# Performance work log

Measured on AMD Instinct MI355X. Metric: run time of the kernel, lower is better.

Reference implementation:

```python
import jax, jax.numpy as jnp
import numpy as np

N = 50000   # nnodes
E = 1600000 # edges (avg degree 32)
F = 128     # nfeatures
D = 64      # output_dim
T = 10      # s2v iterations (default in n2v)


def setup_inputs() -> dict:
    key = jax.random.key(0)
    k_x, k_s, k_d, k_w1, k_w2 = jax.random.split(key, 5)
    x = jax.random.normal(k_x, (N, F), dtype=jnp.float32)
    edge_src = jax.random.randint(k_s, (E,), 0, N, dtype=jnp.int32)
    edge_dst = jax.random.randint(k_d, (E,), 0, N, dtype=jnp.int32)
    # xavier_uniform init as in reset_parameters
    s1 = float(np.sqrt(6.0 / (F + D)))
    s2 = float(np.sqrt(6.0 / (D + D)))
    W1 = jax.random.uniform(k_w1, (D, F), jnp.float32, -s1, s1)
    W2 = jax.random.uniform(k_w2, (D, D), jnp.float32, -s2, s2)
    b1 = jnp.zeros((D,), jnp.float32)
    b2 = jnp.zeros((D,), jnp.float32)
    return {"x": x, "W1": W1, "b1": b1, "W2": W2, "b2": b2,
            "edge_src": edge_src, "edge_dst": edge_dst}


def reference(x, W1, b1, W2, b2, edge_src, edge_dst):
    Wx = x @ W1.T + b1                      # [N, D]

    def step(emb, _):
        # sum of neighbor embeddings: gather sources, segment-sum into dests
        agg = jax.ops.segment_sum(emb[edge_src], edge_dst, num_segments=N)  # [N, D]
        emb_new = jax.nn.relu(Wx + agg @ W2.T + b2)
        return emb_new, None

    emb0 = jnp.zeros((N, D), dtype=x.dtype)
    emb, _ = jax.lax.scan(step, emb0, None, length=T)  # n2v
    # g2v: sum node embeddings into graph embedding
    return emb.sum(axis=0)                  # [D]
```

## Files before the change

### kernel.cpp

```cpp
#include <hip/hip_runtime.h>

#define D 64
#define F 128
#define NBMAX 256
#define DB 128

typedef unsigned int uint;
typedef unsigned short ushort;
typedef short s16x8 __attribute__((ext_vector_type(8)));
typedef float f32x4 __attribute__((ext_vector_type(4)));

__device__ __forceinline__ float bf16lo(uint u) { return __uint_as_float(u << 16); }
__device__ __forceinline__ float bf16hi(uint u) { return __uint_as_float(u & 0xFFFF0000u); }
__device__ __forceinline__ ushort f2bf16(float f) {
    uint u = __float_as_uint(f);
    u += 0x7FFFu + ((u >> 16) & 1u);
    return (ushort)(u >> 16);
}
__device__ __forceinline__ uint pk2bf(float lo, float hi) {
    return (uint)f2bf16(lo) | ((uint)f2bf16(hi) << 16);
}


__global__ __launch_bounds__(256) void bucket_hist(const int* __restrict__ dst,
                                                   int* __restrict__ gb, int E, int nb) {
    __shared__ int h[NBMAX];
    for (int t = threadIdx.x; t < nb; t += 256) h[t] = 0;
    __syncthreads();
    int start = blockIdx.x * 4096;
    int end   = start + 4096 < E ? start + 4096 : E;
    for (int i = start + threadIdx.x; i < end; i += 256)
        atomicAdd(&h[dst[i] >> 8], 1);
    __syncthreads();
    for (int t = threadIdx.x; t < nb; t += 256)
        if (h[t]) atomicAdd(&gb[t], h[t]);
}

__global__ void bucket_scan(const int* __restrict__ gb, int* __restrict__ gboff,
                            int* __restrict__ gcur, int nb) {
    if (threadIdx.x == 0) {
        int s = 0;
        for (int b = 0; b < nb; ++b) { gboff[b] = s; gcur[b] = s; s += gb[b]; }
        gboff[nb] = s;
    }
}

__global__ __launch_bounds__(256) void bucket_scatter(const int* __restrict__ src,
                                                      const int* __restrict__ dst,
                                                      int* __restrict__ gcur,
                                                      int* __restrict__ packed, int E, int nb) {
    __shared__ int h[NBMAX], base[NBMAX], lcur[NBMAX];
    for (int t = threadIdx.x; t < nb; t += 256) h[t] = 0;
    __syncthreads();
    int start = blockIdx.x * 4096;
    int end   = start + 4096 < E ? start + 4096 : E;
    for (int i = start + threadIdx.x; i < end; i += 256)
        atomicAdd(&h[dst[i] >> 8], 1);
    __syncthreads();
    for (int t = threadIdx.x; t < nb; t += 256) {
        base[t] = h[t] ? atomicAdd(&gcur[t], h[t]) : 0;
        lcur[t] = 0;
    }
    __syncthreads();
    for (int i = start + threadIdx.x; i < end; i += 256) {
        int d = dst[i];
        int b = d >> 8;
        int pos = base[b] + atomicAdd(&lcur[b], 1);
        packed[pos] = (src[i] << 8) | (d & 255);
    }
}

__global__ __launch_bounds__(256) void bucket_deg(const int* __restrict__ gboff,
                                                  const int* __restrict__ packed,
                                                  int* __restrict__ deg, int N) {
    __shared__ int h[NBMAX];
    int b = blockIdx.x;
    h[threadIdx.x] = 0;
    __syncthreads();
    int st = gboff[b], en = gboff[b + 1];
    for (int i = st + threadIdx.x; i < en; i += 256)
        atomicAdd(&h[packed[i] & 255], 1);
    __syncthreads();
    int node = (b << 8) + threadIdx.x;
    if (node < N) deg[node] = h[threadIdx.x];
}

__global__ __launch_bounds__(256) void bucket_fill(const int* __restrict__ gboff,
                                                   const int* __restrict__ packed,
                                                   const int* __restrict__ row_ptr,
                                                   const int* __restrict__ rank,
                                                   int* __restrict__ col, int N) {
    __shared__ int lcur[NBMAX];
    int b = blockIdx.x;
    int node = (b << 8) + threadIdx.x;
    lcur[threadIdx.x] = (node < N) ? row_ptr[node] : 0;
    __syncthreads();
    int st = gboff[b], en = gboff[b + 1];
    for (int i = st + threadIdx.x; i < en; i += 256) {
        int p = packed[i];
        int pos = atomicAdd(&lcur[p & 255], 1);
        col[pos] = rank[p >> 8];
    }
}


__global__ void count_deg_kernel(const int* __restrict__ dst, int* __restrict__ deg, int E) {
    int i = blockIdx.x * blockDim.x + threadIdx.x;
    if (i < E) atomicAdd(&deg[dst[i]], 1);
}

__global__ void fill_kernel(const int* __restrict__ src, const int* __restrict__ dst,
                            int* __restrict__ cursor, const int* __restrict__ rank,
                            int* __restrict__ col, int E) {
    int i = blockIdx.x * blockDim.x + threadIdx.x;
    if (i < E) {
        int d_ = dst[i];
        int pos = atomicAdd(&cursor[d_], 1);
        col[pos] = rank[src[i]];
    }
}


__global__ __launch_bounds__(256) void dsort_hist(const int* __restrict__ deg,
                                                  int* __restrict__ dh, int N) {
    __shared__ int h[DB];
    if (threadIdx.x < DB) h[threadIdx.x] = 0;
    __syncthreads();
    int start = blockIdx.x * 4096;
    int end   = start + 4096 < N ? start + 4096 : N;
    for (int i = start + threadIdx.x; i < end; i += 256) {
        int d = deg[i];
        atomicAdd(&h[d < DB - 1 ? d : DB - 1], 1);
    }
    __syncthreads();
    if (threadIdx.x < DB && h[threadIdx.x]) atomicAdd(&dh[threadIdx.x], h[threadIdx.x]);
}

__global__ void dsort_scan(const int* __restrict__ dh, int* __restrict__ dcur) {
    if (threadIdx.x == 0) {
        int s = 0;
        for (int b = 0; b < DB; ++b) { dcur[b] = s; s += dh[b]; }
    }
}

__global__ __launch_bounds__(256) void dsort_scatter(const int* __restrict__ deg,
                                                     int* __restrict__ dcur,
                                                     int* __restrict__ perm,
                                                     int* __restrict__ rank, int N) {
    __shared__ int h[DB], base[DB], lc[DB];
    if (threadIdx.x < DB) h[threadIdx.x] = 0;
    __syncthreads();
    int start = blockIdx.x * 4096;
    int end   = start + 4096 < N ? start + 4096 : N;
    for (int i = start + threadIdx.x; i < end; i += 256) {
        int d = deg[i];
        atomicAdd(&h[d < DB - 1 ? d : DB - 1], 1);
    }
    __syncthreads();
    if (threadIdx.x < DB) {
        base[threadIdx.x] = h[threadIdx.x] ? atomicAdd(&dcur[threadIdx.x], h[threadIdx.x]) : 0;
        lc[threadIdx.x] = 0;
    }
    __syncthreads();
    for (int i = start + threadIdx.x; i < end; i += 256) {
        int d = deg[i];
        int b = d < DB - 1 ? d : DB - 1;
        int pos = base[b] + atomicAdd(&lc[b], 1);
        perm[pos] = i;
        rank[i] = pos;
    }
}


__global__ __launch_bounds__(1024) void scan_kernel(const int* __restrict__ deg,
                                                    int* __restrict__ row_ptr, int n) {
    __shared__ int wsum[16];
    int lane = threadIdx.x & 63;
    int wid  = threadIdx.x >> 6;
    int carry = 0;
    const int CH = 4096;
    for (int base = 0; base < n; base += CH) {
        int i0 = base + (int)threadIdx.x * 4;
        int v0 = (i0     < n) ? deg[i0]     : 0;
        int v1 = (i0 + 1 < n) ? deg[i0 + 1] : 0;
        int v2 = (i0 + 2 < n) ? deg[i0 + 2] : 0;
        int v3 = (i0 + 3 < n) ? deg[i0 + 3] : 0;
        int p0 = v0, p1 = p0 + v1, p2 = p1 + v2, p3 = p2 + v3;
        int tsum = p3;
        int s = tsum;
        #pragma unroll
        for (int off = 1; off < 64; off <<= 1) {
            int t = __shfl_up(s, off);
            if (lane >= off) s += t;
        }
        if (lane == 63) wsum[wid] = s;
        __syncthreads();
        int wbase = 0, chunk_total = 0;
        #pragma unroll
        for (int w = 0; w < 16; ++w) {
            int t = wsum[w];
            chunk_total += t;
            if (w < wid) wbase += t;
        }
        __syncthreads();
        int ex = carry + wbase + (s - tsum);
        if (i0     < n) row_ptr[i0 + 1] = ex + p0;
        if (i0 + 1 < n) row_ptr[i0 + 2] = ex + p1;
        if (i0 + 2 < n) row_ptr[i0 + 3] = ex + p2;
        if (i0 + 3 < n) row_ptr[i0 + 4] = ex + p3;
        carry += chunk_total;
    }
    if (threadIdx.x == 0) row_ptr[0] = 0;
}


__global__ __launch_bounds__(256) void wx_mfma_kernel(const float* __restrict__ x,
                                                      const float* __restrict__ W1,
                                                      const float* __restrict__ b1,
                                                      const float* __restrict__ b2,
                                                      const int* __restrict__ perm,
                                                      float* __restrict__ Wx,
                                                      ushort* __restrict__ emb, int N) {
    int lane = threadIdx.x & 63;
    int wv = blockIdx.x * 4 + (threadIdx.x >> 6);
    int nwaves = gridDim.x * 4;
    int r16 = lane & 15;
    int kg  = lane >> 4;

    s16x8 bf[4][4];
    #pragma unroll
    for (int nt = 0; nt < 4; ++nt) {
        const float* wrow = W1 + (size_t)(nt * 16 + r16) * F;
        #pragma unroll
        for (int ks = 0; ks < 4; ++ks) {
            const float4* p = reinterpret_cast<const float4*>(wrow + ks * 32 + kg * 8);
            float4 f0 = p[0], f1 = p[1];
            union { s16x8 v; uint u[4]; } t;
            t.u[0] = pk2bf(f0.x, f0.y); t.u[1] = pk2bf(f0.z, f0.w);
            t.u[2] = pk2bf(f1.x, f1.y); t.u[3] = pk2bf(f1.z, f1.w);
            bf[nt][ks] = t.v;
        }
    }
    float b1v[4], b2v[4];
    #pragma unroll
    for (int nt = 0; nt < 4; ++nt) {
        b1v[nt] = b1[nt * 16 + r16];
        b2v[nt] = b2[nt * 16 + r16];
    }

    int ntiles = (N + 15) >> 4;
    for (int tile = wv; tile < ntiles; tile += nwaves) {
        int row0 = tile << 4;
        int arow = row0 + r16;
        if (arow >= N) arow = N - 1;
        int orig = perm[arow];
        s16x8 af[4];
        #pragma unroll
        for (int ks = 0; ks < 4; ++ks) {
            const float4* p = reinterpret_cast<const float4*>(x + (size_t)orig * F + ks * 32 + kg * 8);
            float4 f0 = p[0], f1 = p[1];
            union { s16x8 v; uint u[4]; } t;
            t.u[0] = pk2bf(f0.x, f0.y); t.u[1] = pk2bf(f0.z, f0.w);
            t.u[2] = pk2bf(f1.x, f1.y); t.u[3] = pk2bf(f1.z, f1.w);
            af[ks] = t.v;
        }
        #pragma unroll
        for (int nt = 0; nt < 4; ++nt) {
            f32x4 acc = {0.f, 0.f, 0.f, 0.f};
            #pragma unroll
            for (int ks = 0; ks < 4; ++ks)
                acc = __builtin_amdgcn_mfma_f32_16x16x32_bf16(af[ks], bf[nt][ks], acc, 0, 0, 0);
            int outd = nt * 16 + r16;
            #pragma unroll
            for (int r = 0; r < 4; ++r) {
                int node = row0 + kg * 4 + r;
                if (node < N) {
                    float wxv = acc[r] + b1v[nt];
                    Wx[(size_t)node * D + outd] = wxv;
                    float e = wxv + b2v[nt];
                    emb[(size_t)node * D + outd] = f2bf16(e > 0.f ? e : 0.f);
                }
            }
        }
    }
}


__global__ __launch_bounds__(256) void step_kernel(const ushort* __restrict__ emb_in,
                                                   ushort* __restrict__ emb_out,
                                                   const float* __restrict__ Wx,
                                                   const float* __restrict__ W2,
                                                   const float* __restrict__ b2,
                                                   const int* __restrict__ row_ptr,
                                                   const int* __restrict__ col,
                                                   const int* __restrict__ perm, int N) {
    int lane = threadIdx.x & 63;
    int w = threadIdx.x >> 6;
    int r = lane & 15;
    int a = lane >> 4;

    s16x8 af[4][2];
    #pragma unroll
    for (int t = 0; t < 4; ++t)
        #pragma unroll
        for (int f = 0; f < 2; ++f) {
            const float4* p = reinterpret_cast<const float4*>(W2 + (size_t)(t * 16 + r) * D + f * 32 + a * 8);
            float4 f0 = p[0], f1 = p[1];
            union { s16x8 v; uint u[4]; } tt;
            tt.u[0] = pk2bf(f0.x, f0.y); tt.u[1] = pk2bf(f0.z, f0.w);
            tt.u[2] = pk2bf(f1.x, f1.y); tt.u[3] = pk2bf(f1.z, f1.w);
            af[t][f] = tt.v;
        }
    float4 b2v[4];
    #pragma unroll
    for (int t = 0; t < 4; ++t)
        b2v[t] = *reinterpret_cast<const float4*>(b2 + t * 16 + a * 4);

    int ntiles = (N + 15) >> 4;
    int tile = blockIdx.x * 4 + w;
    if (tile >= ntiles) return;

    int rg = tile * 16 + r;
    int rgc = rg < N ? rg : N - 1;
    int node = perm[rgc];
    int rp = row_ptr[node];
    int degr = row_ptr[node + 1] - rp;
    if (rg >= N) degr = 0;
    int maxd = degr;
    #pragma unroll
    for (int off = 1; off < 16; off <<= 1) {
        int o = __shfl_xor(maxd, off);
        maxd = o > maxd ? o : maxd;
    }

    float acc0[8] = {0.f, 0.f, 0.f, 0.f, 0.f, 0.f, 0.f, 0.f};
    float acc1[8] = {0.f, 0.f, 0.f, 0.f, 0.f, 0.f, 0.f, 0.f};

    if (maxd > 0) {
        int u0 = (0 < degr) ? col[rp] : N;
        int u1 = (1 < degr) ? col[rp + 1] : N;
        uint4 q00 = *reinterpret_cast<const uint4*>(emb_in + ((size_t)u0 << 6) + (a << 3));
        uint4 q01 = *reinterpret_cast<const uint4*>(emb_in + ((size_t)u0 << 6) + 32 + (a << 3));
        uint4 q10 = *reinterpret_cast<const uint4*>(emb_in + ((size_t)u1 << 6) + (a << 3));
        uint4 q11 = *reinterpret_cast<const uint4*>(emb_in + ((size_t)u1 << 6) + 32 + (a << 3));
        for (int k = 0; k < maxd; ++k) {
            int un = (k + 2 < degr) ? col[rp + k + 2] : N;
            uint4 p0 = *reinterpret_cast<const uint4*>(emb_in + ((size_t)un << 6) + (a << 3));
            uint4 p1 = *reinterpret_cast<const uint4*>(emb_in + ((size_t)un << 6) + 32 + (a << 3));
            acc0[0] += bf16lo(q00.x); acc0[1] += bf16hi(q00.x);
            acc0[2] += bf16lo(q00.y); acc0[3] += bf16hi(q00.y);
            acc0[4] += bf16lo(q00.z); acc0[5] += bf16hi(q00.z);
            acc0[6] += bf16lo(q00.w); acc0[7] += bf16hi(q00.w);
            acc1[0] += bf16lo(q01.x); acc1[1] += bf16hi(q01.x);
            acc1[2] += bf16lo(q01.y); acc1[3] += bf16hi(q01.y);
            acc1[4] += bf16lo(q01.z); acc1[5] += bf16hi(q01.z);
            acc1[6] += bf16lo(q01.w); acc1[7] += bf16hi(q01.w);
            q00 = q10; q01 = q11; q10 = p0; q11 = p1;
        }
    }

    union { s16x8 v; uint u[4]; } B0, B1;
    B0.u[0] = pk2bf(acc0[0], acc0[1]); B0.u[1] = pk2bf(acc0[2], acc0[3]);
    B0.u[2] = pk2bf(acc0[4], acc0[5]); B0.u[3] = pk2bf(acc0[6], acc0[7]);
    B1.u[0] = pk2bf(acc1[0], acc1[1]); B1.u[1] = pk2bf(acc1[2], acc1[3]);
    B1.u[2] = pk2bf(acc1[4], acc1[5]); B1.u[3] = pk2bf(acc1[6], acc1[7]);

    f32x4 d0 = {0.f, 0.f, 0.f, 0.f}, d1 = {0.f, 0.f, 0.f, 0.f};
    f32x4 d2 = {0.f, 0.f, 0.f, 0.f}, d3 = {0.f, 0.f, 0.f, 0.f};
    d0 = __builtin_amdgcn_mfma_f32_16x16x32_bf16(af[0][0], B0.v, d0, 0, 0, 0);
    d1 = __builtin_amdgcn_mfma_f32_16x16x32_bf16(af[1][0], B0.v, d1, 0, 0, 0);
    d2 = __builtin_amdgcn_mfma_f32_16x16x32_bf16(af[2][0], B0.v, d2, 0, 0, 0);
    d3 = __builtin_amdgcn_mfma_f32_16x16x32_bf16(af[3][0], B0.v, d3, 0, 0, 0);
    d0 = __builtin_amdgcn_mfma_f32_16x16x32_bf16(af[0][1], B1.v, d0, 0, 0, 0);
    d1 = __builtin_amdgcn_mfma_f32_16x16x32_bf16(af[1][1], B1.v, d1, 0, 0, 0);
    d2 = __builtin_amdgcn_mfma_f32_16x16x32_bf16(af[2][1], B1.v, d2, 0, 0, 0);
    d3 = __builtin_amdgcn_mfma_f32_16x16x32_bf16(af[3][1], B1.v, d3, 0, 0, 0);

    if (rg < N) {
        const float* wxp = Wx + ((size_t)rg << 6);
        ushort* op = emb_out + ((size_t)rg << 6);
        #pragma unroll
        for (int t = 0; t < 4; ++t) {
            float4 wx4 = *reinterpret_cast<const float4*>(wxp + t * 16 + a * 4);
            f32x4 dd = (t == 0) ? d0 : (t == 1) ? d1 : (t == 2) ? d2 : d3;
            float e0 = wx4.x + b2v[t].x + dd[0];
            float e1 = wx4.y + b2v[t].y + dd[1];
            float e2 = wx4.z + b2v[t].z + dd[2];
            float e3 = wx4.w + b2v[t].w + dd[3];
            e0 = e0 > 0.f ? e0 : 0.f; e1 = e1 > 0.f ? e1 : 0.f;
            e2 = e2 > 0.f ? e2 : 0.f; e3 = e3 > 0.f ? e3 : 0.f;
            uint2 st;
            st.x = pk2bf(e0, e1);
            st.y = pk2bf(e2, e3);
            *reinterpret_cast<uint2*>(op + t * 16 + a * 4) = st;
        }
    }
}


__global__ __launch_bounds__(256) void reduce_kernel(const ushort* __restrict__ emb,
                                                     float* __restrict__ out, int N) {
    int lane = threadIdx.x & 63;
    int wid  = threadIdx.x >> 6;
    float acc = 0.f;
    int nw = gridDim.x * 4;
    for (int v = blockIdx.x * 4 + wid; v < N; v += nw)
        acc += __uint_as_float((uint)emb[(size_t)v * D + lane] << 16);
    __shared__ float red[256];
    red[threadIdx.x] = acc;
    __syncthreads();
    if (threadIdx.x < 64) {
        float sum = red[threadIdx.x] + red[threadIdx.x + 64] +
                    red[threadIdx.x + 128] + red[threadIdx.x + 192];
        atomicAdd(&out[threadIdx.x], sum);
    }
}

extern "C" void kernel_launch(void* const* d_in, const int* in_sizes, int n_in,
                              void* d_out, int out_size, void* d_ws, size_t ws_size,
                              hipStream_t stream) {
    const float* x    = (const float*)d_in[0];
    const float* W1   = (const float*)d_in[1];
    const float* b1   = (const float*)d_in[2];
    const float* W2   = (const float*)d_in[3];
    const float* b2   = (const float*)d_in[4];
    const int*   esrc = (const int*)d_in[5];
    const int*   edst = (const int*)d_in[6];
    int N = in_sizes[0] / F;
    int E = in_sizes[5];
    float* out = (float*)d_out;

    char* ws = (char*)d_ws;
    size_t off = 0;
    auto alloc = [&](size_t bytes) -> char* {
        char* p = ws + off;
        off += (bytes + 255) & ~(size_t)255;
        return p;
    };
    float*  Wx      = (float*)alloc((size_t)N * D * 4);
    ushort* embA    = (ushort*)alloc(((size_t)N + 1) * D * 2);
    ushort* embB    = (ushort*)alloc(((size_t)N + 1) * D * 2);
    int*    row_ptr = (int*)alloc(((size_t)N + 1) * 4);
    int*    deg     = (int*)alloc((size_t)N * 4);
    int*    col     = (int*)alloc((size_t)E * 4);
    int*    packed  = (int*)alloc((size_t)E * 4);
    int*    perm    = (int*)alloc(((size_t)N + 16) * 4);
    int*    rank    = (int*)alloc((size_t)N * 4);
    int*    gb      = (int*)alloc((NBMAX + 1) * 4);
    int*    gboff   = (int*)alloc((NBMAX + 1) * 4);
    int*    gcur    = (int*)alloc((NBMAX + 1) * 4);
    int*    dh      = (int*)alloc(DB * 4);
    int*    dcur    = (int*)alloc(DB * 4);
    int*    cursor  = (int*)alloc((size_t)N * 4);

    hipMemsetAsync(out, 0, (size_t)out_size * 4, stream);
    hipMemsetAsync(embA + (size_t)N * D, 0, D * 2, stream);
    hipMemsetAsync(embB + (size_t)N * D, 0, D * 2, stream);
    hipMemsetAsync(dh, 0, DB * 4, stream);

    int nb = ((N - 1) >> 8) + 1;
    int nchunksE = (E + 4095) / 4096;
    int nchunksN = (N + 4095) / 4096;
    if (N <= 65536) {
        hipMemsetAsync(gb, 0, (size_t)nb * 4, stream);
        bucket_hist<<<nchunksE, 256, 0, stream>>>(edst, gb, E, nb);
        bucket_scan<<<1, 64, 0, stream>>>(gb, gboff, gcur, nb);
        bucket_scatter<<<nchunksE, 256, 0, stream>>>(esrc, edst, gcur, packed, E, nb);
        bucket_deg<<<nb, 256, 0, stream>>>(gboff, packed, deg, N);
        dsort_hist<<<nchunksN, 256, 0, stream>>>(deg, dh, N);
        dsort_scan<<<1, 64, 0, stream>>>(dh, dcur);
        dsort_scatter<<<nchunksN, 256, 0, stream>>>(deg, dcur, perm, rank, N);
        scan_kernel<<<1, 1024, 0, stream>>>(deg, row_ptr, N);
        bucket_fill<<<nb, 256, 0, stream>>>(gboff, packed, row_ptr, rank, col, N);
    } else {
        hipMemsetAsync(deg, 0, (size_t)N * 4, stream);
        count_deg_kernel<<<(E + 255) / 256, 256, 0, stream>>>(edst, deg, E);
        dsort_hist<<<nchunksN, 256, 0, stream>>>(deg, dh, N);
        dsort_scan<<<1, 64, 0, stream>>>(dh, dcur);
        dsort_scatter<<<nchunksN, 256, 0, stream>>>(deg, dcur, perm, rank, N);
        scan_kernel<<<1, 1024, 0, stream>>>(deg, row_ptr, N);
        hipMemcpyAsync(cursor, row_ptr, (size_t)N * 4, hipMemcpyDeviceToDevice, stream);
        fill_kernel<<<(E + 255) / 256, 256, 0, stream>>>(esrc, edst, cursor, rank, col, E);
    }

    wx_mfma_kernel<<<256, 256, 0, stream>>>(x, W1, b1, b2, perm, Wx, embA, N);

    int ntiles = (N + 15) >> 4;
    int sblocks = (ntiles + 3) / 4;
    ushort* pin = embA;
    ushort* pout = embB;
    for (int t = 1; t < 10; ++t) {
        step_kernel<<<sblocks, 256, 0, stream>>>(pin, pout, Wx, W2, b2, row_ptr, col, perm, N);
        ushort* tmp = pin; pin = pout; pout = tmp;
    }
    reduce_kernel<<<256, 256, 0, stream>>>(pin, out, N);
}
```

Before: 657.7 us.

## Deepen neighbor gather prefetch to 4-wide chunks and reverse tile order

The neighbor aggregation loop now loads four neighbor rows per chunk and prefetches the next chunk while summing the current one, replacing the previous depth-2 rolling prefetch. This puts more memory requests in flight to hide gather latency. The W2/b2 fragment loads are moved after the gather loop to lower register pressure during it. Tiles are processed in reverse order, presumably so high-degree tiles from the degree-sorted permutation start first and load balance improves. Together these raise register use, which may cut occupancy.

```diff
diff --git a/kernel.cpp b/kernel.cpp
--- a/kernel.cpp
+++ b/kernel.cpp
@@ -299,26 +299,9 @@
     int r = lane & 15;
     int a = lane >> 4;
 
-    s16x8 af[4][2];
-    #pragma unroll
-    for (int t = 0; t < 4; ++t)
-        #pragma unroll
-        for (int f = 0; f < 2; ++f) {
-            const float4* p = reinterpret_cast<const float4*>(W2 + (size_t)(t * 16 + r) * D + f * 32 + a * 8);
-            float4 f0 = p[0], f1 = p[1];
-            union { s16x8 v; uint u[4]; } tt;
-            tt.u[0] = pk2bf(f0.x, f0.y); tt.u[1] = pk2bf(f0.z, f0.w);
-            tt.u[2] = pk2bf(f1.x, f1.y); tt.u[3] = pk2bf(f1.z, f1.w);
-            af[t][f] = tt.v;
-        }
-    float4 b2v[4];
-    #pragma unroll
-    for (int t = 0; t < 4; ++t)
-        b2v[t] = *reinterpret_cast<const float4*>(b2 + t * 16 + a * 4);
-
     int ntiles = (N + 15) >> 4;
-    int tile = blockIdx.x * 4 + w;
-    if (tile >= ntiles) return;
+    int tile = ntiles - 1 - (blockIdx.x * 4 + w);
+    if (tile < 0) return;
 
     int rg = tile * 16 + r;
     int rgc = rg < N ? rg : N - 1;
@@ -336,28 +319,61 @@
     float acc0[8] = {0.f, 0.f, 0.f, 0.f, 0.f, 0.f, 0.f, 0.f};
     float acc1[8] = {0.f, 0.f, 0.f, 0.f, 0.f, 0.f, 0.f, 0.f};
 
+    const ushort* base0 = emb_in + (a << 3);
+    const ushort* base1 = emb_in + 32 + (a << 3);
+
     if (maxd > 0) {
-        int u0 = (0 < degr) ? col[rp] : N;
-        int u1 = (1 < degr) ? col[rp + 1] : N;
-        uint4 q00 = *reinterpret_cast<const uint4*>(emb_in + ((size_t)u0 << 6) + (a << 3));
-        uint4 q01 = *reinterpret_cast<const uint4*>(emb_in + ((size_t)u0 << 6) + 32 + (a << 3));
-        uint4 q10 = *reinterpret_cast<const uint4*>(emb_in + ((size_t)u1 << 6) + (a << 3));
-        uint4 q11 = *reinterpret_cast<const uint4*>(emb_in + ((size_t)u1 << 6) + 32 + (a << 3));
-        for (int k = 0; k < maxd; ++k) {
-            int un = (k + 2 < degr) ? col[rp + k + 2] : N;
-            uint4 p0 = *reinterpret_cast<const uint4*>(emb_in + ((size_t)un << 6) + (a << 3));
-            uint4 p1 = *reinterpret_cast<const uint4*>(emb_in + ((size_t)un << 6) + 32 + (a << 3));
-            acc0[0] += bf16lo(q00.x); acc0[1] += bf16hi(q00.x);
-            acc0[2] += bf16lo(q00.y); acc0[3] += bf16hi(q00.y);
-            acc0[4] += bf16lo(q00.z); acc0[5] += bf16hi(q00.z);
-            acc0[6] += bf16lo(q00.w); acc0[7] += bf16hi(q00.w);
-            acc1[0] += bf16lo(q01.x); acc1[1] += bf16hi(q01.x);
-            acc1[2] += bf16lo(q01.y); acc1[3] += bf16hi(q01.y);
-            acc1[4] += bf16lo(q01.z); acc1[5] += bf16hi(q01.z);
-            acc1[6] += bf16lo(q01.w); acc1[7] += bf16hi(q01.w);
-            q00 = q10; q01 = q11; q10 = p0; q11 = p1;
-        }
-    }
+        uint4 c0[4], c1[4];
+        #pragma unroll
+        for (int j = 0; j < 4; ++j) {
+            int u = (j < degr) ? col[rp + j] : N;
+            c0[j] = *reinterpret_cast<const uint4*>(base0 + ((size_t)u << 6));
+            c1[j] = *reinterpret_cast<const uint4*>(base1 + ((size_t)u << 6));
+        }
+        int nch = (maxd + 3) >> 2;
+        for (int c = 0; c < nch; ++c) {
+            uint4 n0[4], n1[4];
+            int kb = (c + 1) << 2;
+            if (c + 1 < nch) {
+                #pragma unroll
+                for (int j = 0; j < 4; ++j) {
+                    int u = (kb + j < degr) ? col[rp + kb + j] : N;
+                    n0[j] = *reinterpret_cast<const uint4*>(base0 + ((size_t)u << 6));
+                    n1[j] = *reinterpret_cast<const uint4*>(base1 + ((size_t)u << 6));
+                }
+            }
+            #pragma unroll
+            for (int j = 0; j < 4; ++j) {
+                acc0[0] += bf16lo(c0[j].x); acc0[1] += bf16hi(c0[j].x);
+                acc0[2] += bf16lo(c0[j].y); acc0[3] += bf16hi(c0[j].y);
+                acc0[4] += bf16lo(c0[j].z); acc0[5] += bf16hi(c0[j].z);
+                acc0[6] += bf16lo(c0[j].w); acc0[7] += bf16hi(c0[j].w);
+                acc1[0] += bf16lo(c1[j].x); acc1[1] += bf16hi(c1[j].x);
+                acc1[2] += bf16lo(c1[j].y); acc1[3] += bf16hi(c1[j].y);
+                acc1[4] += bf16lo(c1[j].z); acc1[5] += bf16hi(c1[j].z);
+                acc1[6] += bf16lo(c1[j].w); acc1[7] += bf16hi(c1[j].w);
+            }
+            #pragma unroll
+            for (int j = 0; j < 4; ++j) { c0[j] = n0[j]; c1[j] = n1[j]; }
+        }
+    }
+
+    s16x8 af[4][2];
+    #pragma unroll
+    for (int t = 0; t < 4; ++t)
+        #pragma unroll
+        for (int f = 0; f < 2; ++f) {
+            const float4* p = reinterpret_cast<const float4*>(W2 + (size_t)(t * 16 + r) * D + f * 32 + a * 8);
+            float4 f0 = p[0], f1 = p[1];
+            union { s16x8 v; uint u[4]; } tt;
+            tt.u[0] = pk2bf(f0.x, f0.y); tt.u[1] = pk2bf(f0.z, f0.w);
+            tt.u[2] = pk2bf(f1.x, f1.y); tt.u[3] = pk2bf(f1.z, f1.w);
+            af[t][f] = tt.v;
+        }
+    float4 b2v[4];
+    #pragma unroll
+    for (int t = 0; t < 4; ++t)
+        b2v[t] = *reinterpret_cast<const float4*>(b2 + t * 16 + a * 4);
 
     union { s16x8 v; uint u[4]; } B0, B1;
     B0.u[0] = pk2bf(acc0[0], acc0[1]); B0.u[1] = pk2bf(acc0[2], acc0[3]);
```

After: 589.4 us. 1.12x faster.
